# Performance work log

Measured on AMD Instinct MI355X. Metric: run time of the kernel, lower is better.

The kernel has to match this reference:

```python
import jax, jax.numpy as jnp
import numpy as np

EMBED_DIM = 512
NUM_HEADS = 8
HEAD_DIM = EMBED_DIM // NUM_HEADS
SCALE = HEAD_DIM ** -0.5
B, N = 4, 2048


def setup_inputs() -> dict:
    key = jax.random.key(0)
    ks = jax.random.split(key, 6)
    x = jax.random.normal(ks[0], (B, N, EMBED_DIM), dtype=jnp.float32)
    mask = jnp.ones((B, N, N), dtype=jnp.int32)
    # nn.Linear params: weight [out, in], bias [out]
    lim_qkv = 1.0 / np.sqrt(EMBED_DIM)
    qkv_w = jax.random.uniform(ks[1], (3 * EMBED_DIM, EMBED_DIM), jnp.float32, -lim_qkv, lim_qkv)
    qkv_b = jax.random.uniform(ks[2], (3 * EMBED_DIM,), jnp.float32, -lim_qkv, lim_qkv)
    proj_w = jax.random.uniform(ks[3], (EMBED_DIM, EMBED_DIM), jnp.float32, -lim_qkv, lim_qkv)
    proj_b = jax.random.uniform(ks[4], (EMBED_DIM,), jnp.float32, -lim_qkv, lim_qkv)
    return {"x": x, "qkv_w": qkv_w, "qkv_b": qkv_b, "proj_w": proj_w, "proj_b": proj_b, "mask": mask}


def reference(x, qkv_w, qkv_b, proj_w, proj_b, mask):
    Bb, Nn, C = x.shape
    qkv = (jnp.einsum('bnc,oc->bno', x, qkv_w) + qkv_b).reshape(Bb, Nn, 3, NUM_HEADS, HEAD_DIM)
    qkv = jnp.transpose(qkv, (2, 0, 3, 1, 4))
    q, k, v = qkv[0], qkv[1], qkv[2]
    # full score matrix [B,H,N,N] (faithful to the unfused original)
    attn = jnp.einsum('bhnd,bhmd->bhnm', q, k) * SCALE
    attn = jnp.where(mask[:, None, :, :] == 0, -jnp.inf, attn)
    attn = jax.nn.softmax(attn, axis=-1)
    out = jnp.einsum('bhnm,bhmd->bhnd', attn, v)
    out = jnp.transpose(out, (0, 2, 1, 3)).reshape(Bb, Nn, C)
    out = jnp.einsum('bnc,oc->bno', out, proj_w) + proj_b
    return out
```

## Files before the change

### kernel.cpp

```cpp
#include <hip/hip_runtime.h>
#include <hip/hip_bf16.h>
#include <stdint.h>

#define NB 4
#define NH 8
#define SEQ 2048
#define HD 64
#define CDIM 512

using bf16 = __hip_bfloat16;
typedef __attribute__((ext_vector_type(8))) short short8;
typedef __attribute__((ext_vector_type(4))) short short4_t;
typedef __attribute__((ext_vector_type(4))) float f32x4;

#define NEG_BIG (-3.0e38f)
#define SOFT_C 0.18033688011112042f

__device__ __forceinline__ short bf16_bits(float x) {
  return __builtin_bit_cast(short, __float2bfloat16(x));
}

__device__ __forceinline__ void gld_lds16(const void* g, void* l) {
  __builtin_amdgcn_global_load_lds(
      (const __attribute__((address_space(1))) unsigned int*)g,
      (__attribute__((address_space(3))) unsigned int*)l, 16, 0, 0);
}

#define X4 1048576
#define Q4 196608
#define P4 65536
__global__ __launch_bounds__(256) void prep_cvt(const float* __restrict__ x,
                                                const float* __restrict__ wq,
                                                const float* __restrict__ wp,
                                                short* __restrict__ xb,
                                                short* __restrict__ wqb,
                                                short* __restrict__ wpb) {
  int idx = blockIdx.x * 256 + threadIdx.x;
  int stride = gridDim.x * 256;
  for (int i = idx; i < X4 + Q4 + P4; i += stride) {
    const float* src; short* dst; int off;
    if (i < X4)            { src = x;  dst = xb;  off = i; }
    else if (i < X4 + Q4)  { src = wq; dst = wqb; off = i - X4; }
    else                   { src = wp; dst = wpb; off = i - X4 - Q4; }
    f32x4 v = *(const f32x4*)(src + (size_t)off * 4);
    short4_t o;
    o[0] = bf16_bits(v[0]); o[1] = bf16_bits(v[1]);
    o[2] = bf16_bits(v[2]); o[3] = bf16_bits(v[3]);
    *(short4_t*)(dst + (size_t)off * 4) = o;
  }
}


__global__ __launch_bounds__(256) void qkv_union(const short* __restrict__ Xb,
                                                 const short* __restrict__ Wb,
                                                 const float* __restrict__ bias,
                                                 const int* __restrict__ mask,
                                                 unsigned long long* __restrict__ bits,
                                                 bf16* __restrict__ q,
                                                 bf16* __restrict__ k,
                                                 bf16* __restrict__ vt) {
  __shared__ short Alds[128][32];
  __shared__ short Blds[128][32];
  const int tid = threadIdx.x;
  const int lane = tid & 63;
  const int w = tid >> 6;

  if (blockIdx.x < 512) {
    int wave_g = blockIdx.x * 4 + w;
#pragma unroll 1
    for (int i = 0; i < 32; i++) {
      size_t c = (size_t)i * 2048 + wave_g;
      size_t base = c * 256;
      int v0 = mask[base + 0 * 64 + lane];
      int v1 = mask[base + 1 * 64 + lane];
      int v2 = mask[base + 2 * 64 + lane];
      int v3 = mask[base + 3 * 64 + lane];
      unsigned long long w0 = __ballot(v0 != 0);
      unsigned long long w1 = __ballot(v1 != 0);
      unsigned long long w2 = __ballot(v2 != 0);
      unsigned long long w3 = __ballot(v3 != 0);
      if (lane == 0) {
        bits[c * 4 + 0] = w0; bits[c * 4 + 1] = w1;
        bits[c * 4 + 2] = w2; bits[c * 4 + 3] = w3;
      }
    }
    return;
  }

  const int g = blockIdx.x - 512;
  const int wm = w >> 1, wn = w & 1;
  const int row0 = (g & 63) * 128;
  const int col0 = (g >> 6) * 128;
  const bool isv = (col0 >= 1024);

  f32x4 acc[4][4] = {};
  const int cl = lane & 15;
  const int quad = lane >> 4;

  const int st_r = lane >> 2;
  const int st_gc = (lane & 3) ^ (st_r & 3);
  const int st_col = st_gc * 8;
  const int fc = (quad ^ (cl & 3)) * 8;

  for (int kk = 0; kk < 512; kk += 32) {
#pragma unroll
    for (int t = 0; t < 2; t++) {
      int R = w * 32 + t * 16;
      gld_lds16(&Xb[(size_t)(row0 + R + st_r) * 512 + kk + st_col], &Alds[R][0]);
      gld_lds16(&Wb[(size_t)(col0 + R + st_r) * 512 + kk + st_col], &Blds[R][0]);
    }
    __syncthreads();
    short8 a[4], b[4];
#pragma unroll
    for (int i = 0; i < 4; i++) a[i] = *(const short8*)&Alds[wm * 64 + i * 16 + cl][fc];
#pragma unroll
    for (int j = 0; j < 4; j++) b[j] = *(const short8*)&Blds[wn * 64 + j * 16 + cl][fc];
    if (!isv) {
#pragma unroll
      for (int i = 0; i < 4; i++)
#pragma unroll
        for (int j = 0; j < 4; j++)
          acc[i][j] = __builtin_amdgcn_mfma_f32_16x16x32_bf16(a[i], b[j], acc[i][j], 0, 0, 0);
    } else {
#pragma unroll
      for (int i = 0; i < 4; i++)
#pragma unroll
        for (int j = 0; j < 4; j++)
          acc[i][j] = __builtin_amdgcn_mfma_f32_16x16x32_bf16(b[j], a[i], acc[i][j], 0, 0, 0);
    }
    __syncthreads();
  }

  if (!isv) {
#pragma unroll
    for (int i = 0; i < 4; i++) {
#pragma unroll
      for (int j = 0; j < 4; j++) {
        int col = col0 + wn * 64 + j * 16 + cl;
        float bv = bias[col];
        int which = col >> 9;
        int c = col & 511;
        int h = c >> 6, d = c & 63;
#pragma unroll
        for (int r = 0; r < 4; r++) {
          int row = row0 + wm * 64 + i * 16 + quad * 4 + r;
          int bb = row >> 11, n = row & 2047;
          float val = acc[i][j][r] + bv;
          size_t bh = (size_t)bb * NH + h;
          if (which == 0)      q[(bh * SEQ + n) * HD + d] = __float2bfloat16(val * SOFT_C);
          else                 k[(bh * SEQ + n) * HD + d] = __float2bfloat16(val);
        }
      }
    }
  } else {
#pragma unroll
    for (int i = 0; i < 4; i++) {
#pragma unroll
      for (int j = 0; j < 4; j++) {
        int nrow = row0 + wm * 64 + i * 16 + cl;
        int bb = nrow >> 11, n = nrow & 2047;
#pragma unroll
        for (int r = 0; r < 4; r++) {
          int col = col0 + wn * 64 + j * 16 + quad * 4 + r;
          float bv = bias[col];
          int c = col & 511;
          int h = c >> 6, d = c & 63;
          float val = acc[i][j][r] + bv;
          size_t bh = (size_t)bb * NH + h;
          vt[(bh * HD + d) * SEQ + n] = __float2bfloat16(val);
        }
      }
    }
  }
}

__global__ __launch_bounds__(256) void flash_attn(const bf16* __restrict__ qg,
                                                  const bf16* __restrict__ kg,
                                                  const bf16* __restrict__ vg,
                                                  const unsigned long long* __restrict__ mbits,
                                                  bf16* __restrict__ attn_out) {
  __shared__ short Klds[64][64];
  __shared__ short Vlds[64][64];
  __shared__ short Plds[4][16][72];
  __shared__ unsigned long long Mlds[64];

  const int tid = threadIdx.x;
  const int lane = tid & 63;
  const int w = tid >> 6;
  const int qt = blockIdx.x;
  const int h = blockIdx.y;
  const int b = blockIdx.z;

  const size_t bh = (size_t)b * NH + h;
  const bf16* qp = qg + bh * SEQ * HD;
  const bf16* kp = kg + bh * SEQ * HD;
  const bf16* vp = vg + bh * HD * SEQ;

  const int cl = lane & 15;
  const int quad = lane >> 4;
  const int koff = quad * 8;
  const int qrow_w = qt * 64 + w * 16;

  const int c0 = ((quad ^ (cl & 7)) * 8);

  const int st_row = lane >> 3;
  const int st_chunk = (lane & 7) ^ st_row;
  const int st_col = st_chunk * 8;

  short8 aq0 = *(const short8*)&qp[(size_t)(qrow_w + cl) * HD + koff];
  short8 aq1 = *(const short8*)&qp[(size_t)(qrow_w + cl) * HD + 32 + koff];

  f32x4 o[4] = {};
  float l_l = 0.f;

  for (int kt = 0; kt < 32; kt++) {
    const int kb = kt * 64;
#pragma unroll
    for (int t = 0; t < 2; t++) {
      int rbase = w * 16 + t * 8;
      gld_lds16(&kp[(size_t)(kb + rbase + st_row) * HD + st_col], &Klds[rbase][0]);
      gld_lds16(&vp[(size_t)(rbase + st_row) * SEQ + kb + st_col], &Vlds[rbase][0]);
    }
    if (tid < 64) Mlds[tid] = mbits[((size_t)b * SEQ + qt * 64 + tid) * (SEQ / 64) + kt];
    __syncthreads();

    f32x4 s[4];
#pragma unroll
    for (int nb = 0; nb < 4; nb++) {
      short8 k0 = *(const short8*)&Klds[nb * 16 + cl][c0];
      short8 k1 = *(const short8*)&Klds[nb * 16 + cl][c0 ^ 32];
      f32x4 z = {0.f, 0.f, 0.f, 0.f};
      z = __builtin_amdgcn_mfma_f32_16x16x32_bf16(k0, aq0, z, 0, 0, 0);
      s[nb] = __builtin_amdgcn_mfma_f32_16x16x32_bf16(k1, aq1, z, 0, 0, 0);
    }

    unsigned long long wd = Mlds[w * 16 + cl];
    if (wd != ~0ULL) {
#pragma unroll
      for (int nb = 0; nb < 4; nb++)
#pragma unroll
        for (int r = 0; r < 4; r++)
          if (!((wd >> (nb * 16 + quad * 4 + r)) & 1ULL)) s[nb][r] = NEG_BIG;
    }

    f32x4 ps4 = {0.f, 0.f, 0.f, 0.f};
#pragma unroll
    for (int nb = 0; nb < 4; nb++) {
#pragma unroll
      for (int r = 0; r < 4; r++) s[nb][r] = __builtin_amdgcn_exp2f(s[nb][r]);
      ps4 += s[nb];
    }
    float ps = (ps4[0] + ps4[1]) + (ps4[2] + ps4[3]);
    ps += __shfl_xor(ps, 16);
    ps += __shfl_xor(ps, 32);
    l_l += ps;

#pragma unroll
    for (int nb = 0; nb < 4; nb++) {
      short4_t pk;
      pk[0] = bf16_bits(s[nb][0]); pk[1] = bf16_bits(s[nb][1]);
      pk[2] = bf16_bits(s[nb][2]); pk[3] = bf16_bits(s[nb][3]);
      *(short4_t*)&Plds[w][cl][nb * 16 + quad * 4] = pk;
    }

#pragma unroll
    for (int ks = 0; ks < 2; ks++) {
      short8 pa = *(const short8*)&Plds[w][cl][ks * 32 + koff];
      const int vc = c0 ^ (ks * 32);
#pragma unroll
      for (int db = 0; db < 4; db++) {
        short8 vb = *(const short8*)&Vlds[db * 16 + cl][vc];
        o[db] = __builtin_amdgcn_mfma_f32_16x16x32_bf16(pa, vb, o[db], 0, 0, 0);
      }
    }
    __syncthreads();
  }

  float inv = 1.0f / l_l;
#pragma unroll
  for (int r = 0; r < 4; r++) {
    float ir = __shfl(inv, (lane & 48) + quad * 4 + r);
    int row = qrow_w + quad * 4 + r;
#pragma unroll
    for (int db = 0; db < 4; db++) {
      float val = o[db][r] * ir;
      attn_out[((size_t)b * SEQ + row) * CDIM + h * 64 + db * 16 + cl] = __float2bfloat16(val);
    }
  }
}

__global__ __launch_bounds__(256) void proj_gemm(const bf16* __restrict__ X,
                                                 const short* __restrict__ Wb,
                                                 const float* __restrict__ bias,
                                                 float* __restrict__ out) {
  __shared__ short Alds[128][32];
  __shared__ short Blds[128][32];
  const int tid = threadIdx.x;
  const int lane = tid & 63;
  const int w = tid >> 6;
  const int wm = w >> 1, wn = w & 1;
  const int row0 = blockIdx.x * 128;
  const int col0 = blockIdx.y * 128;

  f32x4 acc[4][4] = {};
  const int cl = lane & 15;
  const int quad = lane >> 4;

  const int st_r = lane >> 2;
  const int st_gc = (lane & 3) ^ (st_r & 3);
  const int st_col = st_gc * 8;
  const int fc = (quad ^ (cl & 3)) * 8;

  for (int kk = 0; kk < 512; kk += 32) {
#pragma unroll
    for (int t = 0; t < 2; t++) {
      int R = w * 32 + t * 16;
      gld_lds16(&X[(size_t)(row0 + R + st_r) * 512 + kk + st_col], &Alds[R][0]);
      gld_lds16(&Wb[(size_t)(col0 + R + st_r) * 512 + kk + st_col], &Blds[R][0]);
    }
    __syncthreads();
    short8 a[4], b[4];
#pragma unroll
    for (int i = 0; i < 4; i++) a[i] = *(const short8*)&Alds[wm * 64 + i * 16 + cl][fc];
#pragma unroll
    for (int j = 0; j < 4; j++) b[j] = *(const short8*)&Blds[wn * 64 + j * 16 + cl][fc];
#pragma unroll
    for (int i = 0; i < 4; i++)
#pragma unroll
      for (int j = 0; j < 4; j++)
        acc[i][j] = __builtin_amdgcn_mfma_f32_16x16x32_bf16(a[i], b[j], acc[i][j], 0, 0, 0);
    __syncthreads();
  }

#pragma unroll
  for (int i = 0; i < 4; i++) {
#pragma unroll
    for (int j = 0; j < 4; j++) {
      int col = col0 + wn * 64 + j * 16 + cl;
      float bv = bias[col];
#pragma unroll
      for (int r = 0; r < 4; r++) {
        int row = row0 + wm * 64 + i * 16 + quad * 4 + r;
        out[(size_t)row * 512 + col] = acc[i][j][r] + bv;
      }
    }
  }
}

extern "C" void kernel_launch(void* const* d_in, const int* in_sizes, int n_in,
                              void* d_out, int out_size, void* d_ws, size_t ws_size,
                              hipStream_t stream) {
  const float* x      = (const float*)d_in[0];
  const float* qkv_w  = (const float*)d_in[1];
  const float* qkv_b  = (const float*)d_in[2];
  const float* proj_w = (const float*)d_in[3];
  const float* proj_b = (const float*)d_in[4];
  const int*   mask   = (const int*)d_in[5];
  float* out = (float*)d_out;

  char* ws = (char*)d_ws;
  bf16* q    = (bf16*)(ws);
  bf16* k    = (bf16*)(ws + 8388608);
  bf16* vt   = (bf16*)(ws + 16777216);
  bf16* attn = (bf16*)(ws + 25165824);
  short* xb  = (short*)(ws + 25165824);
  unsigned long long* mbits = (unsigned long long*)(ws + 33554432);
  short* wqb = (short*)(ws + 35651584);
  short* wpb = (short*)(ws + 37224448);

  prep_cvt<<<dim3(1280), 256, 0, stream>>>(x, qkv_w, proj_w, xb, wqb, wpb);
  qkv_union<<<dim3(512 + 768), 256, 0, stream>>>(xb, wqb, qkv_b, mask, mbits, q, k, vt);
  flash_attn<<<dim3(SEQ / 64, NH, NB), 256, 0, stream>>>(q, k, vt, mbits, attn);
  proj_gemm<<<dim3(64, 4), 256, 0, stream>>>(attn, wpb, proj_b, out);
}
```

Baseline: 226.6 us.

## Process two 16-row query groups per wave to reuse K/V tiles

Each wave in flash_attn now handles 32 query rows as two 16-row groups, so every block covers 128 queries instead of 64. K and V fragments are read from LDS into registers once per tile and reused by both groups, which halves global K/V traffic and LDS reads per query. The grid shrinks to 512 blocks and per-thread register use grows, which can lower occupancy on a 256-CU part. The Plds scratch buffer is reused serially between the two groups.

```diff
diff --git a/kernel.cpp b/kernel.cpp
--- a/kernel.cpp
+++ b/kernel.cpp
@@ -50,7 +50,6 @@
   }
 }
 
-
 __global__ __launch_bounds__(256) void qkv_union(const short* __restrict__ Xb,
                                                  const short* __restrict__ Wb,
                                                  const float* __restrict__ bias,
@@ -182,7 +181,7 @@
   __shared__ short Klds[64][64];
   __shared__ short Vlds[64][64];
   __shared__ short Plds[4][16][72];
-  __shared__ unsigned long long Mlds[64];
+  __shared__ unsigned long long Mlds[128];
 
   const int tid = threadIdx.x;
   const int lane = tid & 63;
@@ -199,7 +198,7 @@
   const int cl = lane & 15;
   const int quad = lane >> 4;
   const int koff = quad * 8;
-  const int qrow_w = qt * 64 + w * 16;
+  const int qrow_w = qt * 128 + w * 32;
 
   const int c0 = ((quad ^ (cl & 7)) * 8);
 
@@ -207,11 +206,15 @@
   const int st_chunk = (lane & 7) ^ st_row;
   const int st_col = st_chunk * 8;
 
-  short8 aq0 = *(const short8*)&qp[(size_t)(qrow_w + cl) * HD + koff];
-  short8 aq1 = *(const short8*)&qp[(size_t)(qrow_w + cl) * HD + 32 + koff];
-
-  f32x4 o[4] = {};
-  float l_l = 0.f;
+  short8 aq[2][2];
+#pragma unroll
+  for (int g = 0; g < 2; g++) {
+    aq[g][0] = *(const short8*)&qp[(size_t)(qrow_w + g * 16 + cl) * HD + koff];
+    aq[g][1] = *(const short8*)&qp[(size_t)(qrow_w + g * 16 + cl) * HD + 32 + koff];
+  }
+
+  f32x4 o[2][4] = {};
+  float l_l[2] = {0.f, 0.f};
 
   for (int kt = 0; kt < 32; kt++) {
     const int kb = kt * 64;
@@ -221,70 +224,84 @@
       gld_lds16(&kp[(size_t)(kb + rbase + st_row) * HD + st_col], &Klds[rbase][0]);
       gld_lds16(&vp[(size_t)(rbase + st_row) * SEQ + kb + st_col], &Vlds[rbase][0]);
     }
-    if (tid < 64) Mlds[tid] = mbits[((size_t)b * SEQ + qt * 64 + tid) * (SEQ / 64) + kt];
-    __syncthreads();
-
-    f32x4 s[4];
+    if (tid < 128) Mlds[tid] = mbits[((size_t)b * SEQ + qt * 128 + tid) * (SEQ / 64) + kt];
+    __syncthreads();
+
+    short8 k0[4], k1[4], vb[2][4];
 #pragma unroll
     for (int nb = 0; nb < 4; nb++) {
-      short8 k0 = *(const short8*)&Klds[nb * 16 + cl][c0];
-      short8 k1 = *(const short8*)&Klds[nb * 16 + cl][c0 ^ 32];
-      f32x4 z = {0.f, 0.f, 0.f, 0.f};
-      z = __builtin_amdgcn_mfma_f32_16x16x32_bf16(k0, aq0, z, 0, 0, 0);
-      s[nb] = __builtin_amdgcn_mfma_f32_16x16x32_bf16(k1, aq1, z, 0, 0, 0);
-    }
-
-    unsigned long long wd = Mlds[w * 16 + cl];
-    if (wd != ~0ULL) {
+      k0[nb] = *(const short8*)&Klds[nb * 16 + cl][c0];
+      k1[nb] = *(const short8*)&Klds[nb * 16 + cl][c0 ^ 32];
+    }
+#pragma unroll
+    for (int ks = 0; ks < 2; ks++)
+#pragma unroll
+      for (int db = 0; db < 4; db++)
+        vb[ks][db] = *(const short8*)&Vlds[db * 16 + cl][c0 ^ (ks * 32)];
+
+#pragma unroll
+    for (int g = 0; g < 2; g++) {
+      f32x4 s[4];
+#pragma unroll
+      for (int nb = 0; nb < 4; nb++) {
+        f32x4 z = {0.f, 0.f, 0.f, 0.f};
+        z = __builtin_amdgcn_mfma_f32_16x16x32_bf16(k0[nb], aq[g][0], z, 0, 0, 0);
+        s[nb] = __builtin_amdgcn_mfma_f32_16x16x32_bf16(k1[nb], aq[g][1], z, 0, 0, 0);
+      }
+
+      unsigned long long wd = Mlds[w * 32 + g * 16 + cl];
+      if (wd != ~0ULL) {
+#pragma unroll
+        for (int nb = 0; nb < 4; nb++)
+#pragma unroll
+          for (int r = 0; r < 4; r++)
+            if (!((wd >> (nb * 16 + quad * 4 + r)) & 1ULL)) s[nb][r] = NEG_BIG;
+      }
+
+      float ps = 0.f;
 #pragma unroll
       for (int nb = 0; nb < 4; nb++)
 #pragma unroll
-        for (int r = 0; r < 4; r++)
-          if (!((wd >> (nb * 16 + quad * 4 + r)) & 1ULL)) s[nb][r] = NEG_BIG;
-    }
-
-    f32x4 ps4 = {0.f, 0.f, 0.f, 0.f};
-#pragma unroll
-    for (int nb = 0; nb < 4; nb++) {
-#pragma unroll
-      for (int r = 0; r < 4; r++) s[nb][r] = __builtin_amdgcn_exp2f(s[nb][r]);
-      ps4 += s[nb];
-    }
-    float ps = (ps4[0] + ps4[1]) + (ps4[2] + ps4[3]);
-    ps += __shfl_xor(ps, 16);
-    ps += __shfl_xor(ps, 32);
-    l_l += ps;
-
-#pragma unroll
-    for (int nb = 0; nb < 4; nb++) {
-      short4_t pk;
-      pk[0] = bf16_bits(s[nb][0]); pk[1] = bf16_bits(s[nb][1]);
-      pk[2] = bf16_bits(s[nb][2]); pk[3] = bf16_bits(s[nb][3]);
-      *(short4_t*)&Plds[w][cl][nb * 16 + quad * 4] = pk;
-    }
-
-#pragma unroll
-    for (int ks = 0; ks < 2; ks++) {
-      short8 pa = *(const short8*)&Plds[w][cl][ks * 32 + koff];
-      const int vc = c0 ^ (ks * 32);
+        for (int r = 0; r < 4; r++) {
+          float p = __builtin_amdgcn_exp2f(s[nb][r]);
+          s[nb][r] = p;
+          ps += p;
+        }
+      ps += __shfl_xor(ps, 16);
+      ps += __shfl_xor(ps, 32);
+      l_l[g] += ps;
+
+#pragma unroll
+      for (int nb = 0; nb < 4; nb++) {
+        short4_t pk;
+        pk[0] = bf16_bits(s[nb][0]); pk[1] = bf16_bits(s[nb][1]);
+        pk[2] = bf16_bits(s[nb][2]); pk[3] = bf16_bits(s[nb][3]);
+        *(short4_t*)&Plds[w][cl][nb * 16 + quad * 4] = pk;
+      }
+
+#pragma unroll
+      for (int ks = 0; ks < 2; ks++) {
+        short8 pa = *(const short8*)&Plds[w][cl][ks * 32 + koff];
+#pragma unroll
+        for (int db = 0; db < 4; db++)
+          o[g][db] = __builtin_amdgcn_mfma_f32_16x16x32_bf16(pa, vb[ks][db], o[g][db], 0, 0, 0);
+      }
+    }
+    __syncthreads();
+  }
+
+#pragma unroll
+  for (int g = 0; g < 2; g++) {
+    float inv = 1.0f / l_l[g];
+#pragma unroll
+    for (int r = 0; r < 4; r++) {
+      float ir = __shfl(inv, (lane & 48) + quad * 4 + r);
+      int row = qrow_w + g * 16 + quad * 4 + r;
 #pragma unroll
       for (int db = 0; db < 4; db++) {
-        short8 vb = *(const short8*)&Vlds[db * 16 + cl][vc];
-        o[db] = __builtin_amdgcn_mfma_f32_16x16x32_bf16(pa, vb, o[db], 0, 0, 0);
-      }
-    }
-    __syncthreads();
-  }
-
-  float inv = 1.0f / l_l;
-#pragma unroll
-  for (int r = 0; r < 4; r++) {
-    float ir = __shfl(inv, (lane & 48) + quad * 4 + r);
-    int row = qrow_w + quad * 4 + r;
-#pragma unroll
-    for (int db = 0; db < 4; db++) {
-      float val = o[db][r] * ir;
-      attn_out[((size_t)b * SEQ + row) * CDIM + h * 64 + db * 16 + cl] = __float2bfloat16(val);
+        float val = o[g][db][r] * ir;
+        attn_out[((size_t)b * SEQ + row) * CDIM + h * 64 + db * 16 + cl] = __float2bfloat16(val);
+      }
     }
   }
 }
@@ -370,6 +387,6 @@
 
   prep_cvt<<<dim3(1280), 256, 0, stream>>>(x, qkv_w, proj_w, xb, wqb, wpb);
   qkv_union<<<dim3(512 + 768), 256, 0, stream>>>(xb, wqb, qkv_b, mask, mbits, q, k, vt);
-  flash_attn<<<dim3(SEQ / 64, NH, NB), 256, 0, stream>>>(q, k, vt, mbits, attn);
+  flash_attn<<<dim3(SEQ / 128, NH, NB), 256, 0, stream>>>(q, k, vt, mbits, attn);
   proj_gemm<<<dim3(64, 4), 256, 0, stream>>>(attn, wpb, proj_b, out);
 }
```

New measurement: 228.9 us. Within noise of the previous version (+1.0%).
